# Kernel tuning notes

Hardware: AMD Instinct MI355X
Metric: run time of the kernel (lower is better)

The kernel has to match this reference:

```python
import jax, jax.numpy as jnp
import numpy as np

EMBED_DIM = 1024
NUM_HEADS = 16
HEAD_DIM = EMBED_DIM // NUM_HEADS


def setup_inputs() -> dict:
    key = jax.random.key(0)
    ks = jax.random.split(key, 5)
    B, S, E = 2, 2048, EMBED_DIM
    # xavier-uniform-ish scale for square linear weights
    lim = float(np.sqrt(6.0 / (E + E)))
    x = jax.random.normal(ks[0], (B, S, E), dtype=jnp.float32)
    Wq = jax.random.uniform(ks[1], (E, E), jnp.float32, -lim, lim)
    Wk = jax.random.uniform(ks[2], (E, E), jnp.float32, -lim, lim)
    Wv = jax.random.uniform(ks[3], (E, E), jnp.float32, -lim, lim)
    Wo = jax.random.uniform(ks[4], (E, E), jnp.float32, -lim, lim)
    z = jnp.zeros((E,), jnp.float32)
    return {"x": x, "Wq": Wq, "bq": z, "Wk": Wk, "bk": z,
            "Wv": Wv, "bv": z, "Wo": Wo, "bo": z}


def reference(x, Wq, bq, Wk, bk, Wv, bv, Wo, bo):
    B, S, E = x.shape
    H, Dh = NUM_HEADS, HEAD_DIM
    # Linear projections (torch Linear: y = x @ W.T + b)
    q = (x @ Wq.T + bq).reshape(B, S, H, Dh).transpose(0, 2, 1, 3)  # [B,H,S,Dh]
    k = (x @ Wk.T + bk).reshape(B, S, H, Dh).transpose(0, 2, 1, 3)
    v = (x @ Wv.T + bv).reshape(B, S, H, Dh).transpose(0, 2, 1, 3)
    # NOTE: module scales by 1/head_dim (not 1/sqrt(head_dim)) — faithful.
    logits = jnp.einsum('bhqd,bhkd->bhqk', q, k) / Dh  # [B,H,S,S]
    attn = jax.nn.softmax(logits, axis=-1)
    vals = jnp.einsum('bhqk,bhkd->bhqd', attn, v)      # [B,H,S,Dh]
    vals = vals.transpose(0, 2, 1, 3).reshape(B, S, E)
    out = vals @ Wo.T + bo
    return out
```

## Files before the change

### kernel.cpp

```cpp
#include <hip/hip_runtime.h>
#include <hip/hip_bf16.h>

#define EDIM 1024
#define NH   16
#define DH   64
#define BB   2
#define SS   2048
#define MM   (BB*SS)

typedef unsigned short u16;
typedef unsigned int   u32;
typedef __attribute__((ext_vector_type(4)))  float f32x4;
typedef __attribute__((ext_vector_type(16))) float f32x16;
typedef __attribute__((ext_vector_type(8)))  short s16x8;

__device__ __forceinline__ u16 f2bf(float x) {
    __hip_bfloat16 b = __float2bfloat16(x);
    return *(u16*)&b;
}
__device__ __forceinline__ u32 cvtpk(float lo, float hi_) {
    u32 r;
    asm("v_cvt_pk_bf16_f32 %0, %1, %2" : "=v"(r) : "v"(lo), "v"(hi_));
    return r;
}
__device__ __forceinline__ void swap32(u32& a, u32& b) {
    asm("v_permlane32_swap_b32 %0, %1" : "+v"(a), "+v"(b));
}

__device__ __forceinline__ void gload16(const void* g, void* l) {
    __builtin_amdgcn_global_load_lds(
        (const __attribute__((address_space(1))) unsigned int*)g,
        (__attribute__((address_space(3))) unsigned int*)l, 16, 0, 0);
}

__global__ __launch_bounds__(256) void convert_all(const float* __restrict__ x,
                                                   const float* __restrict__ Wq,
                                                   const float* __restrict__ Wk,
                                                   const float* __restrict__ Wv,
                                                   const float* __restrict__ Wo,
                                                   u16* __restrict__ xh,
                                                   u16* __restrict__ wqkv,
                                                   u16* __restrict__ woh)
{
    const int i = blockIdx.x * 256 + threadIdx.x;
    const float* src; ushort4* dst; int off;
    if (i < 1048576)      { src = x;  dst = (ushort4*)xh;   off = i; }
    else if (i < 1310720) { src = Wq; dst = (ushort4*)wqkv; off = i - 1048576; }
    else if (i < 1572864) { src = Wk; dst = (ushort4*)wqkv; off = i - 1310720 + 262144; }
    else if (i < 1835008) { src = Wv; dst = (ushort4*)wqkv; off = i - 1572864 + 524288; }
    else                  { src = Wo; dst = (ushort4*)woh;  off = i - 1835008; }
    const int so = (i < 1048576) ? i
                 : (i < 1310720) ? (i - 1048576)
                 : (i < 1572864) ? (i - 1310720)
                 : (i < 1835008) ? (i - 1572864) : (i - 1835008);
    const float4 v = ((const float4*)src)[so];
    ushort4 h;
    h.x = f2bf(v.x); h.y = f2bf(v.y); h.z = f2bf(v.z); h.w = f2bf(v.w);
    dst[off] = h;
}

__global__ __launch_bounds__(256) void gemm_qkv(const u16* __restrict__ A,
                                                const u16* __restrict__ B,
                                                const float* __restrict__ bq,
                                                const float* __restrict__ bk,
                                                const float* __restrict__ bv,
                                                u16* __restrict__ qb,
                                                u16* __restrict__ kb,
                                                u16* __restrict__ vT)
{
    __shared__ __align__(16) u16 As[128][64];
    __shared__ __align__(16) u16 Bs[128][64];

    const int tid  = threadIdx.x;
    const int lane = tid & 63, wid = tid >> 6;
    const int wm = wid >> 1, wn = wid & 1;
    const int swz = (blockIdx.x & 7) * 96 + (blockIdx.x >> 3);
    const int m0 = (swz & 31) * 128;
    const int n0 = (swz >> 5) * 128;

    size_t aoff[4], boff[4];
    #pragma unroll
    for (int i = 0; i < 4; ++i) {
        const int flat = i * 256 + tid;
        const int row = flat >> 3, u = flat & 7;
        const size_t o = (size_t)row * 2048 + ((u ^ (row & 7)) << 4);
        aoff[i] = o; boff[i] = o;
    }
    const char* Abase = (const char*)(A + (size_t)m0 * 1024);
    const char* Bbase = (const char*)(B + (size_t)n0 * 1024);

    f32x4 acc[4][4];
    #pragma unroll
    for (int i = 0; i < 4; ++i)
        #pragma unroll
        for (int j = 0; j < 4; ++j) acc[i][j] = f32x4{0.f, 0.f, 0.f, 0.f};

    #pragma unroll 1
    for (int t = 0; t < 16; ++t) {
        const size_t kb_ = (size_t)t * 128;
        #pragma unroll
        for (int i = 0; i < 4; ++i)
            gload16(Abase + aoff[i] + kb_, (char*)As + (i * 256 + wid * 64) * 16);
        #pragma unroll
        for (int i = 0; i < 4; ++i)
            gload16(Bbase + boff[i] + kb_, (char*)Bs + (i * 256 + wid * 64) * 16);
        __syncthreads();

        #pragma unroll
        for (int kk = 0; kk < 2; ++kk) {
            s16x8 af[4], bfr[4];
            #pragma unroll
            for (int i = 0; i < 4; ++i) {
                const int rowA = wm * 64 + i * 16 + (lane & 15);
                af[i] = *(const s16x8*)((const char*)As + rowA * 128 + (((kk * 4 + (lane >> 4)) ^ (rowA & 7)) << 4));
                const int rowB = wn * 64 + i * 16 + (lane & 15);
                bfr[i] = *(const s16x8*)((const char*)Bs + rowB * 128 + (((kk * 4 + (lane >> 4)) ^ (rowB & 7)) << 4));
            }
            #pragma unroll
            for (int i = 0; i < 4; ++i)
                #pragma unroll
                for (int j = 0; j < 4; ++j)
                    acc[i][j] = __builtin_amdgcn_mfma_f32_16x16x32_bf16(af[i], bfr[j], acc[i][j], 0, 0, 0);
        }
        __syncthreads();
    }

    if (n0 < 1024) {
        #pragma unroll
        for (int i = 0; i < 4; ++i) {
            const int mbase = m0 + wm * 64 + i * 16 + ((lane >> 4) * 4);
            #pragma unroll
            for (int j = 0; j < 4; ++j) {
                const int n = n0 + wn * 64 + j * 16 + (lane & 15);
                const float bias = bq[n];
                const int h_ = n >> 6, d_ = n & 63;
                #pragma unroll
                for (int r = 0; r < 4; ++r) {
                    const int m = mbase + r;
                    const int b_ = m >> 11, s_ = m & 2047;
                    qb[((size_t)(b_ * NH + h_) * SS + s_) * DH + d_] = f2bf(acc[i][j][r] + bias);
                }
            }
        }
    } else if (n0 < 2048) {
        #pragma unroll
        for (int i = 0; i < 4; ++i) {
            const int mbase = m0 + wm * 64 + i * 16 + ((lane >> 4) * 4);
            #pragma unroll
            for (int j = 0; j < 4; ++j) {
                const int n = n0 + wn * 64 + j * 16 + (lane & 15);
                const float bias = bk[n - 1024];
                const int h_ = (n >> 6) & 15, d_ = n & 63;
                #pragma unroll
                for (int r = 0; r < 4; ++r) {
                    const int m = mbase + r;
                    const int b_ = m >> 11, s_ = m & 2047;
                    kb[((size_t)(b_ * NH + h_) * SS + s_) * DH + d_] = f2bf(acc[i][j][r] + bias);
                }
            }
        }
    } else {
        #pragma unroll
        for (int i = 0; i < 4; ++i) {
            const int mbase = m0 + wm * 64 + i * 16 + ((lane >> 4) * 4);
            #pragma unroll
            for (int j = 0; j < 4; ++j) {
                const int n = n0 + wn * 64 + j * 16 + (lane & 15);
                const float bias = bv[n - 2048];
                const int hd = n - 2048;
                #pragma unroll
                for (int r = 0; r < 4; ++r) {
                    const int m = mbase + r;
                    const int b_ = m >> 11, s_ = m & 2047;
                    vT[((size_t)(b_ * EDIM) + hd) * SS + s_] = f2bf(acc[i][j][r] + bias);
                }
            }
        }
    }
}

__global__ __launch_bounds__(256) void gemm_out(const u16* __restrict__ A,
                                                const u16* __restrict__ B,
                                                const float* __restrict__ bo,
                                                float* __restrict__ out)
{
    __shared__ __align__(16) u16 As[64][64];
    __shared__ __align__(16) u16 Bs[128][64];

    const int tid  = threadIdx.x;
    const int lane = tid & 63, wid = tid >> 6;
    const int wm = wid >> 1, wn = wid & 1;
    const int swz = (blockIdx.x & 7) * 64 + (blockIdx.x >> 3);
    const int m0 = (swz & 63) * 64;
    const int n0 = (swz >> 6) * 128;

    size_t aoff[2], boff[4];
    #pragma unroll
    for (int i = 0; i < 2; ++i) {
        const int flat = i * 256 + tid;
        const int row = flat >> 3, u = flat & 7;
        aoff[i] = (size_t)row * 2048 + ((u ^ (row & 7)) << 4);
    }
    #pragma unroll
    for (int i = 0; i < 4; ++i) {
        const int flat = i * 256 + tid;
        const int row = flat >> 3, u = flat & 7;
        boff[i] = (size_t)row * 2048 + ((u ^ (row & 7)) << 4);
    }
    const char* Abase = (const char*)(A + (size_t)m0 * 1024);
    const char* Bbase = (const char*)(B + (size_t)n0 * 1024);

    f32x4 acc[2][4];
    #pragma unroll
    for (int i = 0; i < 2; ++i)
        #pragma unroll
        for (int j = 0; j < 4; ++j) acc[i][j] = f32x4{0.f, 0.f, 0.f, 0.f};

    #pragma unroll 1
    for (int t = 0; t < 16; ++t) {
        const size_t kb_ = (size_t)t * 128;
        #pragma unroll
        for (int i = 0; i < 2; ++i)
            gload16(Abase + aoff[i] + kb_, (char*)As + (i * 256 + wid * 64) * 16);
        #pragma unroll
        for (int i = 0; i < 4; ++i)
            gload16(Bbase + boff[i] + kb_, (char*)Bs + (i * 256 + wid * 64) * 16);
        __syncthreads();

        #pragma unroll
        for (int kk = 0; kk < 2; ++kk) {
            s16x8 af[2], bfr[4];
            #pragma unroll
            for (int i = 0; i < 2; ++i) {
                const int rowA = wm * 32 + i * 16 + (lane & 15);
                af[i] = *(const s16x8*)((const char*)As + rowA * 128 + (((kk * 4 + (lane >> 4)) ^ (rowA & 7)) << 4));
            }
            #pragma unroll
            for (int j = 0; j < 4; ++j) {
                const int rowB = wn * 64 + j * 16 + (lane & 15);
                bfr[j] = *(const s16x8*)((const char*)Bs + rowB * 128 + (((kk * 4 + (lane >> 4)) ^ (rowB & 7)) << 4));
            }
            #pragma unroll
            for (int i = 0; i < 2; ++i)
                #pragma unroll
                for (int j = 0; j < 4; ++j)
                    acc[i][j] = __builtin_amdgcn_mfma_f32_16x16x32_bf16(af[i], bfr[j], acc[i][j], 0, 0, 0);
        }
        __syncthreads();
    }

    #pragma unroll
    for (int i = 0; i < 2; ++i) {
        const int mbase = m0 + wm * 32 + i * 16 + ((lane >> 4) * 4);
        #pragma unroll
        for (int j = 0; j < 4; ++j) {
            const int n = n0 + wn * 64 + j * 16 + (lane & 15);
            #pragma unroll
            for (int r = 0; r < 4; ++r)
                out[(size_t)(mbase + r) * EDIM + n] = acc[i][j][r] + bo[n];
        }
    }
}

__global__ __launch_bounds__(256) void attn_mfma(const u16* __restrict__ q,
                                                 const u16* __restrict__ k,
                                                 const u16* __restrict__ vT,
                                                 u16* __restrict__ valsh)
{
    __shared__ __align__(16) u16 kt[2][128][64];
    __shared__ __align__(16) u16 vt[2][64][128];

    const int tid = threadIdx.x, lane = tid & 63, wid = tid >> 6;
    const int lq = lane & 31, hi = lane >> 5;
    const int swz = (blockIdx.x & 7) * 64 + (blockIdx.x >> 3);
    const int bh = swz >> 4, qt = swz & 15;
    const int b = bh >> 4, h = bh & 15;

    const u16* qg = q + ((size_t)bh * SS + qt * 128 + wid * 32 + lq) * DH + hi * 8;
    s16x8 qf[4];
    #pragma unroll
    for (int ks = 0; ks < 4; ++ks) qf[ks] = *(const s16x8*)(qg + ks * 16);

    f32x16 acc_o[2];
    #pragma unroll
    for (int db = 0; db < 2; ++db)
        #pragma unroll
        for (int r = 0; r < 16; ++r) acc_o[db][r] = 0.f;
    float rs = 0.f;

    const char* kbh = (const char*)(k + (size_t)bh * SS * DH);
    const char* vbh = (const char*)(vT + ((size_t)b * EDIM + h * DH) * SS);

    auto stage = [&](int buf, int c0) {
        #pragma unroll
        for (int i = 0; i < 4; ++i) {
            const int flat = i * 256 + tid;
            const int row = flat >> 3, u = flat & 7;
            const int su = u ^ (row & 7) ^ ((row >> 3) & 3);
            gload16(kbh + (size_t)(c0 + row) * 128 + (su << 4),
                    (char*)kt + buf * 16384 + (i * 256 + wid * 64) * 16);
        }
        #pragma unroll
        for (int i = 0; i < 4; ++i) {
            const int flat = i * 256 + tid;
            const int row = flat >> 4, u = flat & 15;
            const int su = u ^ (row & 15) ^ ((row & 16) >> 2);
            gload16(vbh + (size_t)row * (SS * 2) + (size_t)c0 * 2 + (su << 4),
                    (char*)vt + buf * 16384 + (i * 256 + wid * 64) * 16);
        }
    };

    stage(0, 0);
    __syncthreads();

    int buf = 0;
    #pragma unroll 1
    for (int c = 0; c < 16; ++c) {
        if (c < 15) stage(buf ^ 1, (c + 1) * 128);
        const char* ktb = (const char*)kt + buf * 16384;
        const char* vtb = (const char*)vt + buf * 16384;

        #pragma unroll
        for (int kb = 0; kb < 4; ++kb) {
            f32x16 sc;
            #pragma unroll
            for (int r = 0; r < 16; ++r) sc[r] = 0.f;
            const int krow = kb * 32 + lq;
            #pragma unroll
            for (int ks = 0; ks < 4; ++ks) {
                const int u = (ks * 2 + hi) ^ (krow & 7) ^ ((krow >> 3) & 3);
                const s16x8 kf = *(const s16x8*)(ktb + krow * 128 + u * 16);
                sc = __builtin_amdgcn_mfma_f32_32x32x16_bf16(kf, qf[ks], sc, 0, 0, 0);
            }

            #pragma unroll
            for (int r = 0; r < 16; ++r) {
                sc[r] = __builtin_amdgcn_exp2f(sc[r] * 0.0225421209f);
                rs += sc[r];
            }

            u32 w0 = cvtpk(sc[0],  sc[1]),  w1 = cvtpk(sc[2],  sc[3]);
            u32 w2 = cvtpk(sc[4],  sc[5]),  w3 = cvtpk(sc[6],  sc[7]);
            u32 w4 = cvtpk(sc[8],  sc[9]),  w5 = cvtpk(sc[10], sc[11]);
            u32 w6 = cvtpk(sc[12], sc[13]), w7 = cvtpk(sc[14], sc[15]);
            swap32(w0, w2);
            swap32(w1, w3);
            swap32(w4, w6);
            swap32(w5, w7);
            union { u32 w[4]; s16x8 v; } pa0, pa1;
            pa0.w[0] = w0; pa0.w[1] = w1; pa0.w[2] = w2; pa0.w[3] = w3;
            pa1.w[0] = w4; pa1.w[1] = w5; pa1.w[2] = w6; pa1.w[3] = w7;

            #pragma unroll
            for (int t = 0; t < 2; ++t) {
                const s16x8 pat = t ? pa1.v : pa0.v;
                const int kst = kb * 2 + t;
                #pragma unroll
                for (int db = 0; db < 2; ++db) {
                    const int vrow = db * 32 + lq;
                    const int u = (kst * 2 + hi) ^ (vrow & 15) ^ ((vrow & 16) >> 2);
                    const s16x8 vf = *(const s16x8*)(vtb + vrow * 256 + u * 16);
                    acc_o[db] = __builtin_amdgcn_mfma_f32_32x32x16_bf16(pat, vf, acc_o[db], 0, 0, 0);
                }
            }
        }
        __syncthreads();
        buf ^= 1;
    }

    const float rsf = rs + __shfl_xor(rs, 32, 64);
    const float inv = 1.f / rsf;
    float iv[16];
    #pragma unroll
    for (int r = 0; r < 16; ++r)
        iv[r] = __shfl(inv, (r & 3) + 8 * (r >> 2) + 4 * hi, 64);

    #pragma unroll
    for (int db = 0; db < 2; ++db)
        #pragma unroll
        for (int r = 0; r < 16; ++r) {
            const int srow = qt * 128 + wid * 32 + (r & 3) + 8 * (r >> 2) + 4 * hi;
            const int col  = h * 64 + db * 32 + lq;
            valsh[(size_t)(b * SS + srow) * EDIM + col] = f2bf(acc_o[db][r] * iv[r]);
        }
}

extern "C" void kernel_launch(void* const* d_in, const int* in_sizes, int n_in,
                              void* d_out, int out_size, void* d_ws, size_t ws_size,
                              hipStream_t stream)
{
    const float* x  = (const float*)d_in[0];
    const float* Wq = (const float*)d_in[1];
    const float* bq = (const float*)d_in[2];
    const float* Wk = (const float*)d_in[3];
    const float* bk = (const float*)d_in[4];
    const float* Wv = (const float*)d_in[5];
    const float* bv = (const float*)d_in[6];
    const float* Wo = (const float*)d_in[7];
    const float* bo = (const float*)d_in[8];
    float* out = (float*)d_out;

    u16* W = (u16*)d_ws;
    const size_t M1 = 1024 * 1024;
    u16* xh    = W;
    u16* wqkv  = W + 4  * M1;
    u16* woh   = W + 7  * M1;
    u16* qbuf  = W + 8  * M1;
    u16* kbuf  = W + 12 * M1;
    u16* vbufT = W + 16 * M1;
    u16* valsh = W + 20 * M1;

    convert_all<<<dim3(8192), 256, 0, stream>>>(x, Wq, Wk, Wv, Wo, xh, wqkv, woh);

    gemm_qkv<<<dim3(768), 256, 0, stream>>>(xh, wqkv, bq, bk, bv, qbuf, kbuf, vbufT);

    attn_mfma<<<dim3(BB * NH * (SS / 128)), 256, 0, stream>>>(qbuf, kbuf, vbufT, valsh);

    gemm_out<<<dim3(512), 256, 0, stream>>>(valsh, woh, bo, out);
}
```

Baseline: 206.6 us.

## Single-buffer attention LDS, fold softmax scale into Q, add MFMA priority hints

The attention kernel drops double-buffered K/V staging in favor of a single LDS buffer that is loaded and then synchronized at the start of each chunk. This halves LDS use, which may allow more resident blocks, but load latency is no longer overlapped with compute within a block. The softmax scale is folded into the Q projection epilogue, removing a multiply per score. s_setprio raises wave priority around the MFMA sections to favor matrix issue across co-resident waves.

```diff
diff --git a/kernel.cpp b/kernel.cpp
--- a/kernel.cpp
+++ b/kernel.cpp
@@ -32,6 +32,8 @@
         (const __attribute__((address_space(1))) unsigned int*)g,
         (__attribute__((address_space(3))) unsigned int*)l, 16, 0, 0);
 }
+
+#define QSCALE 0.0225421209f
 
 __global__ __launch_bounds__(256) void convert_all(const float* __restrict__ x,
                                                    const float* __restrict__ Wq,
@@ -138,7 +140,8 @@
                 for (int r = 0; r < 4; ++r) {
                     const int m = mbase + r;
                     const int b_ = m >> 11, s_ = m & 2047;
-                    qb[((size_t)(b_ * NH + h_) * SS + s_) * DH + d_] = f2bf(acc[i][j][r] + bias);
+                    qb[((size_t)(b_ * NH + h_) * SS + s_) * DH + d_] =
+                        f2bf((acc[i][j][r] + bias) * QSCALE);
                 }
             }
         }
@@ -267,8 +270,8 @@
                                                  const u16* __restrict__ vT,
                                                  u16* __restrict__ valsh)
 {
-    __shared__ __align__(16) u16 kt[2][128][64];
-    __shared__ __align__(16) u16 vt[2][64][128];
+    __shared__ __align__(16) u16 kt[128][64];
+    __shared__ __align__(16) u16 vt[64][128];
 
     const int tid = threadIdx.x, lane = tid & 63, wid = tid >> 6;
     const int lq = lane & 31, hi = lane >> 5;
@@ -290,35 +293,31 @@
 
     const char* kbh = (const char*)(k + (size_t)bh * SS * DH);
     const char* vbh = (const char*)(vT + ((size_t)b * EDIM + h * DH) * SS);
-
-    auto stage = [&](int buf, int c0) {
-        #pragma unroll
-        for (int i = 0; i < 4; ++i) {
-            const int flat = i * 256 + tid;
-            const int row = flat >> 3, u = flat & 7;
-            const int su = u ^ (row & 7) ^ ((row >> 3) & 3);
-            gload16(kbh + (size_t)(c0 + row) * 128 + (su << 4),
-                    (char*)kt + buf * 16384 + (i * 256 + wid * 64) * 16);
-        }
-        #pragma unroll
-        for (int i = 0; i < 4; ++i) {
-            const int flat = i * 256 + tid;
-            const int row = flat >> 4, u = flat & 15;
-            const int su = u ^ (row & 15) ^ ((row & 16) >> 2);
-            gload16(vbh + (size_t)row * (SS * 2) + (size_t)c0 * 2 + (su << 4),
-                    (char*)vt + buf * 16384 + (i * 256 + wid * 64) * 16);
-        }
-    };
-
-    stage(0, 0);
-    __syncthreads();
-
-    int buf = 0;
+    const char* ksrc[4]; const char* vsrc[4];
+    #pragma unroll
+    for (int i = 0; i < 4; ++i) {
+        const int flat = i * 256 + tid;
+        const int row = flat >> 3, u = flat & 7;
+        const int su = u ^ (row & 7) ^ ((row >> 3) & 3);
+        ksrc[i] = kbh + (size_t)row * 128 + (su << 4);
+        const int rowv = flat >> 4, uv = flat & 15;
+        const int suv = uv ^ (rowv & 15) ^ ((rowv & 16) >> 2);
+        vsrc[i] = vbh + (size_t)rowv * (SS * 2) + (suv << 4);
+    }
+
     #pragma unroll 1
     for (int c = 0; c < 16; ++c) {
-        if (c < 15) stage(buf ^ 1, (c + 1) * 128);
-        const char* ktb = (const char*)kt + buf * 16384;
-        const char* vtb = (const char*)vt + buf * 16384;
+        #pragma unroll
+        for (int i = 0; i < 4; ++i) {
+            gload16(ksrc[i], (char*)kt + (i * 256 + wid * 64) * 16);
+            ksrc[i] += 128 * 128;
+        }
+        #pragma unroll
+        for (int i = 0; i < 4; ++i) {
+            gload16(vsrc[i], (char*)vt + (i * 256 + wid * 64) * 16);
+            vsrc[i] += 256;
+        }
+        __syncthreads();
 
         #pragma unroll
         for (int kb = 0; kb < 4; ++kb) {
@@ -326,16 +325,18 @@
             #pragma unroll
             for (int r = 0; r < 16; ++r) sc[r] = 0.f;
             const int krow = kb * 32 + lq;
+            __builtin_amdgcn_s_setprio(1);
             #pragma unroll
             for (int ks = 0; ks < 4; ++ks) {
                 const int u = (ks * 2 + hi) ^ (krow & 7) ^ ((krow >> 3) & 3);
-                const s16x8 kf = *(const s16x8*)(ktb + krow * 128 + u * 16);
+                const s16x8 kf = *(const s16x8*)((const char*)kt + krow * 128 + u * 16);
                 sc = __builtin_amdgcn_mfma_f32_32x32x16_bf16(kf, qf[ks], sc, 0, 0, 0);
             }
+            __builtin_amdgcn_s_setprio(0);
 
             #pragma unroll
             for (int r = 0; r < 16; ++r) {
-                sc[r] = __builtin_amdgcn_exp2f(sc[r] * 0.0225421209f);
+                sc[r] = __builtin_amdgcn_exp2f(sc[r]);
                 rs += sc[r];
             }
 
@@ -351,6 +352,7 @@
             pa0.w[0] = w0; pa0.w[1] = w1; pa0.w[2] = w2; pa0.w[3] = w3;
             pa1.w[0] = w4; pa1.w[1] = w5; pa1.w[2] = w6; pa1.w[3] = w7;
 
+            __builtin_amdgcn_s_setprio(1);
             #pragma unroll
             for (int t = 0; t < 2; ++t) {
                 const s16x8 pat = t ? pa1.v : pa0.v;
@@ -359,13 +361,13 @@
                 for (int db = 0; db < 2; ++db) {
                     const int vrow = db * 32 + lq;
                     const int u = (kst * 2 + hi) ^ (vrow & 15) ^ ((vrow & 16) >> 2);
-                    const s16x8 vf = *(const s16x8*)(vtb + vrow * 256 + u * 16);
+                    const s16x8 vf = *(const s16x8*)((const char*)vt + vrow * 256 + u * 16);
                     acc_o[db] = __builtin_amdgcn_mfma_f32_32x32x16_bf16(pat, vf, acc_o[db], 0, 0, 0);
                 }
             }
-        }
-        __syncthreads();
-        buf ^= 1;
+            __builtin_amdgcn_s_setprio(0);
+        }
+        __syncthreads();
     }
 
     const float rsf = rs + __shfl_xor(rs, 32, 64);
```

After: 200.0 us. 1.03x faster.
